# Kernel tuning notes

Hardware: AMD Instinct MI355X
Metric: run time of the kernel (lower is better)

## Reference

```python
import jax, jax.numpy as jnp
import numpy as np


def setup_inputs() -> dict:
    key = jax.random.key(0)
    k1, k2, k3, k4 = jax.random.split(key, 4)
    N, F, E = 100000, 128, 1600000
    Fo = F // 2
    x = jax.random.normal(k1, (N, F), dtype=jnp.float32)
    edge_index = jax.random.randint(k2, (2, E), 0, N, dtype=jnp.int32)
    W_conv = jax.random.normal(k3, (Fo, F), dtype=jnp.float32) * (1.0 / np.sqrt(F))
    b_conv = jnp.zeros((Fo,), dtype=jnp.float32)
    W_lin = jax.random.normal(k4, (1, Fo), dtype=jnp.float32) * (1.0 / np.sqrt(Fo))
    b_lin = jnp.zeros((1,), dtype=jnp.float32)
    return {"x": x, "edge_index": edge_index, "W_conv": W_conv,
            "b_conv": b_conv, "W_lin": W_lin, "b_lin": b_lin}


def gcn_conv(x, edge_index, W_conv, b_conv):
    # PyG GCNConv: add self-loops, symmetric normalization, x@W.T, scatter-add, + bias
    N = x.shape[0]
    loops = jnp.arange(N, dtype=edge_index.dtype)
    src = jnp.concatenate([edge_index[0], loops])  # message sources
    dst = jnp.concatenate([edge_index[1], loops])  # aggregation targets
    h = x @ W_conv.T  # [N, Fo]
    deg = jax.ops.segment_sum(jnp.ones_like(dst, dtype=h.dtype), dst, num_segments=N)
    dinv = jnp.where(deg > 0, jax.lax.rsqrt(deg), 0.0)
    norm = dinv[src] * dinv[dst]  # [E+N]
    msg = h[src] * norm[:, None]  # [E+N, Fo] -- dominant memory traffic
    agg = jax.ops.segment_sum(msg, dst, num_segments=N)
    return agg + b_conv


def reference(x, edge_index, W_conv, b_conv, W_lin, b_lin):
    h = gcn_conv(x, edge_index, W_conv, b_conv)
    h = jax.nn.relu(h)
    logits = h @ W_lin.T + b_lin  # [N, 1]
    return jax.nn.sigmoid(logits)
```

## Files before the change

kernel.cpp:

```cpp
#include <hip/hip_runtime.h>
#include <hip/hip_bf16.h>
#include <math.h>

#define F_IN   128
#define F_OUT  64
#define CHUNK  4096
#define EPT    16
#define BSH    7
#define CAP    3072
#define NBCA   1024

typedef short bf16x8 __attribute__((ext_vector_type(8)));
typedef float f32x4  __attribute__((ext_vector_type(4)));

__device__ __forceinline__ unsigned short f2bf(float f) {
    union { float f; unsigned int i; } c; c.f = f;
    unsigned int r = c.i + 0x7FFFu + ((c.i >> 16) & 1u);
    return (unsigned short)(r >> 16);
}
__device__ __forceinline__ unsigned int pk2bf(float a, float b) {
    __hip_bfloat162 p = __float22bfloat162_rn(make_float2(a, b));
    union { __hip_bfloat162 h; unsigned int u; } c; c.h = p; return c.u;
}
__device__ __forceinline__ float u_lo(unsigned int u) {
    union { unsigned int i; float f; } c; c.i = u << 16; return c.f;
}
__device__ __forceinline__ float u_hi(unsigned int u) {
    union { unsigned int i; float f; } c; c.i = u & 0xFFFF0000u; return c.f;
}

__global__ __launch_bounds__(256) void k_bin(
    const int* __restrict__ src, const int* __restrict__ dst, int E,
    unsigned int* __restrict__ bcnt, unsigned int* __restrict__ entries, int NBC) {
    __shared__ int hist[NBCA];
    __shared__ int gbase[NBCA];
    __shared__ int lcur[NBCA];
    const int tid = threadIdx.x;
    const int e0 = blockIdx.x * CHUNK;

    for (int c = tid; c < NBCA; c += 256) { hist[c] = 0; lcur[c] = 0; }
    __syncthreads();

    int dv[EPT], sv[EPT];
    #pragma unroll
    for (int j = 0; j < EPT; ++j) {
        int e = e0 + j * 256 + tid;
        if (e < E) {
            dv[j] = dst[e];
            sv[j] = src[e];
            atomicAdd(&hist[dv[j] >> BSH], 1);
        } else dv[j] = -1;
    }
    __syncthreads();

    for (int c = tid; c < NBC; c += 256) {
        int h = hist[c];
        gbase[c] = h ? (int)atomicAdd(&bcnt[c], (unsigned int)h) : 0;
    }
    __syncthreads();

    #pragma unroll
    for (int j = 0; j < EPT; ++j) {
        if (dv[j] >= 0) {
            int b = dv[j] >> BSH;
            int r = atomicAdd(&lcur[b], 1);
            entries[b * CAP + gbase[b] + r] =
                ((unsigned int)(dv[j] & 127) << 24) | (unsigned int)sv[j];
        }
    }
}

__global__ __launch_bounds__(256) void k_sort(
    const unsigned int* __restrict__ entries, const unsigned int* __restrict__ bcnt,
    int2* __restrict__ od, unsigned int* __restrict__ srcs, int N) {
    __shared__ unsigned int le[CAP];
    __shared__ unsigned int ls[CAP];
    __shared__ int hist[128];
    __shared__ int curs[128];
    const int tid = threadIdx.x;
    const int b = blockIdx.x;
    const int base = b * CAP;
    const int cnt = min((int)bcnt[b], CAP);

    if (tid < 128) hist[tid] = 0;
    __syncthreads();
    for (int i = tid; i < cnt; i += 256) {
        unsigned int v = entries[base + i];
        le[i] = v;
        atomicAdd(&hist[v >> 24], 1);
    }
    __syncthreads();

    int cntv = (tid < 128) ? hist[tid] : 0;
    if (tid < 128) curs[tid] = cntv;
    __syncthreads();
    for (int off = 1; off < 128; off <<= 1) {
        int t = (tid >= off && tid < 128) ? curs[tid - off] : 0;
        __syncthreads();
        if (tid < 128) curs[tid] += t;
        __syncthreads();
    }
    if (tid < 128) {
        int excl = curs[tid] - cntv;
        int d = (b << BSH) + tid;
        if (d < N) od[d] = make_int2(base + excl, cntv);
        curs[tid] = excl;
    }
    __syncthreads();

    for (int i = tid; i < cnt; i += 256) {
        unsigned int v = le[i];
        int p = atomicAdd(&curs[v >> 24], 1);
        ls[p] = (v & 0xFFFFFFu) << 7;
    }
    __syncthreads();

    for (int i = tid; i < cnt; i += 256)
        srcs[base + i] = ls[i];
}

__global__ __launch_bounds__(256) void k_gemm(
    const float* __restrict__ x, const float* __restrict__ W,
    const int2* __restrict__ od, unsigned short* __restrict__ g, int N) {
    __shared__ unsigned short xs[64 * F_IN];
    __shared__ unsigned short Wsh[F_OUT * F_IN];
    __shared__ float dinvs[64];

    const int tid  = threadIdx.x;
    const int row0 = blockIdx.x * 64;

    {
        const float4* W4 = (const float4*)W;
        #pragma unroll
        for (int t = 0; t < 8; ++t) {
            int idx = t * 256 + tid;
            float4 v = W4[idx];
            uint2 u = make_uint2(pk2bf(v.x, v.y), pk2bf(v.z, v.w));
            *(uint2*)&Wsh[idx * 4] = u;
        }
    }
    {
        const float4* x4 = (const float4*)x;
        #pragma unroll
        for (int t = 0; t < 8; ++t) {
            int idx = t * 256 + tid;
            int r = idx >> 5;
            int grow = row0 + r;
            float4 v = make_float4(0.f, 0.f, 0.f, 0.f);
            if (grow < N) v = x4[(size_t)grow * 32 + (idx & 31)];
            uint2 u = make_uint2(pk2bf(v.x, v.y), pk2bf(v.z, v.w));
            *(uint2*)&xs[idx * 4] = u;
        }
    }
    if (tid < 64) {
        int grow = row0 + tid;
        float dv = 1.0f;
        if (grow < N) dv = rsqrtf((float)od[grow].y + 1.0f);
        dinvs[tid] = dv;
    }
    __syncthreads();

    const int lane = tid & 63;
    const int wave = tid >> 6;
    const int m = lane & 15;
    const int q = lane >> 4;
    const int r0 = wave * 16;

    bf16x8 a[4];
    #pragma unroll
    for (int ks = 0; ks < 4; ++ks)
        a[ks] = *(const bf16x8*)&xs[(r0 + m) * F_IN + ks * 32 + q * 8];

    f32x4 acc[4] = {{0,0,0,0},{0,0,0,0},{0,0,0,0},{0,0,0,0}};
    #pragma unroll
    for (int ct = 0; ct < 4; ++ct) {
        #pragma unroll
        for (int ks = 0; ks < 4; ++ks) {
            bf16x8 b = *(const bf16x8*)&Wsh[(ct * 16 + m) * F_IN + ks * 32 + q * 8];
            acc[ct] = __builtin_amdgcn_mfma_f32_16x16x32_bf16(a[ks], b, acc[ct], 0, 0, 0);
        }
    }

    float dv[4];
    #pragma unroll
    for (int reg = 0; reg < 4; ++reg)
        dv[reg] = dinvs[r0 + q * 4 + reg];
    #pragma unroll
    for (int ct = 0; ct < 4; ++ct) {
        #pragma unroll
        for (int reg = 0; reg < 4; ++reg) {
            int grow = row0 + r0 + q * 4 + reg;
            if (grow <= N)
                g[(size_t)grow * F_OUT + ct * 16 + m] = f2bf(acc[ct][reg] * dv[reg]);
        }
    }
}

__global__ __launch_bounds__(256) void k_pull(
    const unsigned short* __restrict__ g, const int2* __restrict__ od,
    const unsigned int* __restrict__ srcs,
    const float* __restrict__ b_conv, const float* __restrict__ W_lin,
    const float* __restrict__ b_lin, float* __restrict__ out, int N) {
    const int lane = threadIdx.x & 63;
    const int li   = lane & 15;
    const int grp  = lane >> 4;
    const int wave   = (blockIdx.x * blockDim.x + threadIdx.x) >> 6;
    const int nwaves = (gridDim.x * blockDim.x) >> 6;

    const float4 wl = ((const float4*)W_lin)[li];
    const float4 bb = ((const float4*)b_conv)[li];
    const float  bl = b_lin[0];
    const char* gb = (const char*)g;
    const unsigned int lioff = ((unsigned int)li) << 3;
    const unsigned int sentb = ((unsigned int)N) << 7;

    for (int i = wave; i < N; i += nwaves) {
        int2 odv = od[i];
        int e0 = __builtin_amdgcn_readfirstlane(odv.x);
        int dg = __builtin_amdgcn_readfirstlane(odv.y);
        int full = dg >> 4;
        int rem  = dg & 15;

        uint2 us = *(const uint2*)(gb + ((((unsigned int)i) << 7) | lioff));
        float4 acc;
        acc.x = grp ? 0.f : u_lo(us.x);
        acc.y = grp ? 0.f : u_hi(us.x);
        acc.z = grp ? 0.f : u_lo(us.y);
        acc.w = grp ? 0.f : u_hi(us.y);

        const unsigned int* sp = srcs + e0 + grp;
        for (int it = 0; it < full; ++it) {
            unsigned int off[4];
            #pragma unroll
            for (int t = 0; t < 4; ++t)
                off[t] = sp[4 * t];
            uint2 u[4];
            #pragma unroll
            for (int t = 0; t < 4; ++t)
                u[t] = *(const uint2*)(gb + (size_t)(off[t] | lioff));
            #pragma unroll
            for (int t = 0; t < 4; ++t) {
                acc.x += u_lo(u[t].x); acc.y += u_hi(u[t].x);
                acc.z += u_lo(u[t].y); acc.w += u_hi(u[t].y);
            }
            sp += 16;
        }
        if (rem) {
            unsigned int off[4];
            #pragma unroll
            for (int t = 0; t < 4; ++t) {
                unsigned int o = sp[4 * t];
                off[t] = (4 * t + grp < rem) ? o : sentb;
            }
            uint2 u[4];
            #pragma unroll
            for (int t = 0; t < 4; ++t)
                u[t] = *(const uint2*)(gb + (size_t)(off[t] | lioff));
            #pragma unroll
            for (int t = 0; t < 4; ++t) {
                acc.x += u_lo(u[t].x); acc.y += u_hi(u[t].x);
                acc.z += u_lo(u[t].y); acc.w += u_hi(u[t].y);
            }
        }

        #pragma unroll
        for (int mk = 16; mk <= 32; mk <<= 1) {
            acc.x += __shfl_xor(acc.x, mk, 64);
            acc.y += __shfl_xor(acc.y, mk, 64);
            acc.z += __shfl_xor(acc.z, mk, 64);
            acc.w += __shfl_xor(acc.w, mk, 64);
        }

        float dinv = rsqrtf((float)dg + 1.0f);
        float r0 = fmaxf(acc.x * dinv + bb.x, 0.f);
        float r1 = fmaxf(acc.y * dinv + bb.y, 0.f);
        float r2 = fmaxf(acc.z * dinv + bb.z, 0.f);
        float r3 = fmaxf(acc.w * dinv + bb.w, 0.f);
        float t = r0 * wl.x + r1 * wl.y + r2 * wl.z + r3 * wl.w;
        #pragma unroll
        for (int mk = 1; mk <= 8; mk <<= 1)
            t += __shfl_xor(t, mk, 64);
        if (lane == 0)
            out[i] = 1.0f / (1.0f + expf(-(t + bl)));
    }
}

extern "C" void kernel_launch(void* const* d_in, const int* in_sizes, int n_in,
                              void* d_out, int out_size, void* d_ws, size_t ws_size,
                              hipStream_t stream) {
    const float* x      = (const float*)d_in[0];
    const int*   ei     = (const int*)d_in[1];
    const float* W_conv = (const float*)d_in[2];
    const float* b_conv = (const float*)d_in[3];
    const float* W_lin  = (const float*)d_in[4];
    const float* b_lin  = (const float*)d_in[5];

    const int N = in_sizes[0] / F_IN;
    const int E = in_sizes[1] / 2;
    const int* src = ei;
    const int* dst = ei + E;
    float* out = (float*)d_out;

    const int NBC  = (N + 127) >> BSH;
    const int NBLK = (E + CHUNK - 1) / CHUNK;
    const int Na   = NBC << BSH;

    unsigned int* bcnt = (unsigned int*)d_ws;
    int2* od = (int2*)(bcnt + NBCA);
    unsigned int* entries = (unsigned int*)((int*)od + 2 * Na);
    unsigned int* srcs = entries + (size_t)NBC * CAP;
    char* graw = (char*)(srcs + (size_t)NBC * CAP + 64);
    unsigned short* g = (unsigned short*)(((size_t)graw + 255) & ~(size_t)255);

    hipMemsetAsync(bcnt, 0, NBCA * 4, stream);
    k_bin  <<<NBLK, 256, 0, stream>>>(src, dst, E, bcnt, entries, NBC);
    k_sort <<<NBC, 256, 0, stream>>>(entries, bcnt, od, srcs, N);
    k_gemm <<<(N + 64) / 64, 256, 0, stream>>>(x, W_conv, od, g, N);
    k_pull <<<4096, 256, 0, stream>>>(g, od, srcs, b_conv, W_lin, b_lin, out, N);
}
```

Measured before the change: 175.9 us.

## Fuse bin, sort, gemm and pull stages into one cooperative persistent kernel

Merges the four separate launches into a single cooperative kernel that runs each stage as a grid-stride loop and separates stages with grid-wide barriers. It keeps the old multi-kernel path as a fallback if the cooperative launch fails. The binning chunk size is halved so the persistent grid spreads the work more evenly. The goal is to remove launch gaps and tail effects between kernels, at the cost of lower occupancy, grid-sync overhead and a single shared-memory footprint sized for the largest stage.

```diff
diff --git a/kernel.cpp b/kernel.cpp
--- a/kernel.cpp
+++ b/kernel.cpp
@@ -1,14 +1,17 @@
 #include <hip/hip_runtime.h>
+#include <hip/hip_cooperative_groups.h>
 #include <hip/hip_bf16.h>
 #include <math.h>
 
 #define F_IN   128
 #define F_OUT  64
-#define CHUNK  4096
-#define EPT    16
 #define BSH    7
 #define CAP    3072
-#define NBCA   1024
+#define CHUNK  2048
+#define EPT    8
+#define SMEM_SZ 33024
+
+namespace cg = cooperative_groups;
 
 typedef short bf16x8 __attribute__((ext_vector_type(8)));
 typedef float f32x4  __attribute__((ext_vector_type(4)));
@@ -29,174 +32,170 @@
     union { unsigned int i; float f; } c; c.i = u & 0xFFFF0000u; return c.f;
 }
 
-__global__ __launch_bounds__(256) void k_bin(
+__device__ __forceinline__ void dev_bin(
     const int* __restrict__ src, const int* __restrict__ dst, int E,
-    unsigned int* __restrict__ bcnt, unsigned int* __restrict__ entries, int NBC) {
-    __shared__ int hist[NBCA];
-    __shared__ int gbase[NBCA];
-    __shared__ int lcur[NBCA];
+    int NBC, int NCHUNK,
+    unsigned int* __restrict__ bcnt, unsigned int* __restrict__ entries,
+    char* smem) {
+    int* hist  = (int*)smem;
+    int* gbase = hist + 1024;
+    int* lcur  = gbase + 1024;
     const int tid = threadIdx.x;
-    const int e0 = blockIdx.x * CHUNK;
-
-    for (int c = tid; c < NBCA; c += 256) { hist[c] = 0; lcur[c] = 0; }
-    __syncthreads();
-
-    int dv[EPT], sv[EPT];
-    #pragma unroll
-    for (int j = 0; j < EPT; ++j) {
-        int e = e0 + j * 256 + tid;
-        if (e < E) {
-            dv[j] = dst[e];
-            sv[j] = src[e];
-            atomicAdd(&hist[dv[j] >> BSH], 1);
-        } else dv[j] = -1;
-    }
-    __syncthreads();
-
-    for (int c = tid; c < NBC; c += 256) {
-        int h = hist[c];
-        gbase[c] = h ? (int)atomicAdd(&bcnt[c], (unsigned int)h) : 0;
-    }
-    __syncthreads();
-
-    #pragma unroll
-    for (int j = 0; j < EPT; ++j) {
-        if (dv[j] >= 0) {
-            int b = dv[j] >> BSH;
-            int r = atomicAdd(&lcur[b], 1);
-            entries[b * CAP + gbase[b] + r] =
-                ((unsigned int)(dv[j] & 127) << 24) | (unsigned int)sv[j];
-        }
-    }
-}
-
-__global__ __launch_bounds__(256) void k_sort(
+    for (int c = blockIdx.x; c < NCHUNK; c += gridDim.x) {
+        for (int i = tid; i < 1024; i += 256) { hist[i] = 0; lcur[i] = 0; }
+        __syncthreads();
+        const int e0 = c * CHUNK;
+        int dv[EPT], sv[EPT];
+        #pragma unroll
+        for (int j = 0; j < EPT; ++j) {
+            int e = e0 + j * 256 + tid;
+            if (e < E) {
+                dv[j] = dst[e];
+                sv[j] = src[e];
+                atomicAdd(&hist[dv[j] >> BSH], 1);
+            } else dv[j] = -1;
+        }
+        __syncthreads();
+        for (int b = tid; b < NBC; b += 256) {
+            int h = hist[b];
+            gbase[b] = h ? (int)atomicAdd(&bcnt[b], (unsigned int)h) : 0;
+        }
+        __syncthreads();
+        #pragma unroll
+        for (int j = 0; j < EPT; ++j) {
+            if (dv[j] >= 0) {
+                int b = dv[j] >> BSH;
+                int r = atomicAdd(&lcur[b], 1);
+                entries[b * CAP + gbase[b] + r] =
+                    ((unsigned int)(dv[j] & 127) << 24) | (unsigned int)sv[j];
+            }
+        }
+        __syncthreads();
+    }
+}
+
+__device__ __forceinline__ void dev_sort(
     const unsigned int* __restrict__ entries, const unsigned int* __restrict__ bcnt,
-    int2* __restrict__ od, unsigned int* __restrict__ srcs, int N) {
-    __shared__ unsigned int le[CAP];
-    __shared__ unsigned int ls[CAP];
-    __shared__ int hist[128];
-    __shared__ int curs[128];
+    int2* __restrict__ od, unsigned int* __restrict__ srcs, int N, int NBC,
+    char* smem) {
+    unsigned int* le = (unsigned int*)smem;
+    unsigned int* ls = le + CAP;
+    int* hist = (int*)(ls + CAP);
+    int* curs = hist + 128;
     const int tid = threadIdx.x;
-    const int b = blockIdx.x;
-    const int base = b * CAP;
-    const int cnt = min((int)bcnt[b], CAP);
-
-    if (tid < 128) hist[tid] = 0;
-    __syncthreads();
-    for (int i = tid; i < cnt; i += 256) {
-        unsigned int v = entries[base + i];
-        le[i] = v;
-        atomicAdd(&hist[v >> 24], 1);
-    }
-    __syncthreads();
-
-    int cntv = (tid < 128) ? hist[tid] : 0;
-    if (tid < 128) curs[tid] = cntv;
-    __syncthreads();
-    for (int off = 1; off < 128; off <<= 1) {
-        int t = (tid >= off && tid < 128) ? curs[tid - off] : 0;
-        __syncthreads();
-        if (tid < 128) curs[tid] += t;
-        __syncthreads();
-    }
-    if (tid < 128) {
-        int excl = curs[tid] - cntv;
-        int d = (b << BSH) + tid;
-        if (d < N) od[d] = make_int2(base + excl, cntv);
-        curs[tid] = excl;
-    }
-    __syncthreads();
-
-    for (int i = tid; i < cnt; i += 256) {
-        unsigned int v = le[i];
-        int p = atomicAdd(&curs[v >> 24], 1);
-        ls[p] = (v & 0xFFFFFFu) << 7;
-    }
-    __syncthreads();
-
-    for (int i = tid; i < cnt; i += 256)
-        srcs[base + i] = ls[i];
-}
-
-__global__ __launch_bounds__(256) void k_gemm(
+    for (int b = blockIdx.x; b < NBC; b += gridDim.x) {
+        const int base = b * CAP;
+        const int cnt = min((int)bcnt[b], CAP);
+        if (tid < 128) hist[tid] = 0;
+        __syncthreads();
+        for (int i = tid; i < cnt; i += 256) {
+            unsigned int v = entries[base + i];
+            le[i] = v;
+            atomicAdd(&hist[v >> 24], 1);
+        }
+        __syncthreads();
+        int cntv = (tid < 128) ? hist[tid] : 0;
+        if (tid < 128) curs[tid] = cntv;
+        __syncthreads();
+        for (int off = 1; off < 128; off <<= 1) {
+            int t = (tid >= off && tid < 128) ? curs[tid - off] : 0;
+            __syncthreads();
+            if (tid < 128) curs[tid] += t;
+            __syncthreads();
+        }
+        if (tid < 128) {
+            int excl = curs[tid] - cntv;
+            int d = (b << BSH) + tid;
+            if (d < N) od[d] = make_int2(base + excl, cntv);
+            curs[tid] = excl;
+        }
+        __syncthreads();
+        for (int i = tid; i < cnt; i += 256) {
+            unsigned int v = le[i];
+            int p = atomicAdd(&curs[v >> 24], 1);
+            ls[p] = (v & 0xFFFFFFu) << 7;
+        }
+        __syncthreads();
+        for (int i = tid; i < cnt; i += 256)
+            srcs[base + i] = ls[i];
+        __syncthreads();
+    }
+}
+
+__device__ __forceinline__ void dev_gemm(
     const float* __restrict__ x, const float* __restrict__ W,
-    const int2* __restrict__ od, unsigned short* __restrict__ g, int N) {
-    __shared__ unsigned short xs[64 * F_IN];
-    __shared__ unsigned short Wsh[F_OUT * F_IN];
-    __shared__ float dinvs[64];
-
-    const int tid  = threadIdx.x;
-    const int row0 = blockIdx.x * 64;
-
+    const int2* __restrict__ od, unsigned short* __restrict__ g, int N, int NT,
+    char* smem) {
+    unsigned short* xs  = (unsigned short*)smem;
+    unsigned short* Wsh = xs + 64 * F_IN;
+    float* dinvs = (float*)(Wsh + F_OUT * F_IN);
+    const int tid = threadIdx.x;
     {
         const float4* W4 = (const float4*)W;
         #pragma unroll
         for (int t = 0; t < 8; ++t) {
             int idx = t * 256 + tid;
             float4 v = W4[idx];
-            uint2 u = make_uint2(pk2bf(v.x, v.y), pk2bf(v.z, v.w));
-            *(uint2*)&Wsh[idx * 4] = u;
-        }
-    }
-    {
-        const float4* x4 = (const float4*)x;
-        #pragma unroll
-        for (int t = 0; t < 8; ++t) {
-            int idx = t * 256 + tid;
-            int r = idx >> 5;
-            int grow = row0 + r;
-            float4 v = make_float4(0.f, 0.f, 0.f, 0.f);
-            if (grow < N) v = x4[(size_t)grow * 32 + (idx & 31)];
-            uint2 u = make_uint2(pk2bf(v.x, v.y), pk2bf(v.z, v.w));
-            *(uint2*)&xs[idx * 4] = u;
-        }
-    }
-    if (tid < 64) {
-        int grow = row0 + tid;
-        float dv = 1.0f;
-        if (grow < N) dv = rsqrtf((float)od[grow].y + 1.0f);
-        dinvs[tid] = dv;
-    }
-    __syncthreads();
-
+            *(uint2*)&Wsh[idx * 4] = make_uint2(pk2bf(v.x, v.y), pk2bf(v.z, v.w));
+        }
+    }
     const int lane = tid & 63;
-    const int wave = tid >> 6;
+    const int wv = tid >> 6;
     const int m = lane & 15;
     const int q = lane >> 4;
-    const int r0 = wave * 16;
-
-    bf16x8 a[4];
-    #pragma unroll
-    for (int ks = 0; ks < 4; ++ks)
-        a[ks] = *(const bf16x8*)&xs[(r0 + m) * F_IN + ks * 32 + q * 8];
-
-    f32x4 acc[4] = {{0,0,0,0},{0,0,0,0},{0,0,0,0},{0,0,0,0}};
-    #pragma unroll
-    for (int ct = 0; ct < 4; ++ct) {
-        #pragma unroll
-        for (int ks = 0; ks < 4; ++ks) {
-            bf16x8 b = *(const bf16x8*)&Wsh[(ct * 16 + m) * F_IN + ks * 32 + q * 8];
-            acc[ct] = __builtin_amdgcn_mfma_f32_16x16x32_bf16(a[ks], b, acc[ct], 0, 0, 0);
-        }
-    }
-
-    float dv[4];
-    #pragma unroll
-    for (int reg = 0; reg < 4; ++reg)
-        dv[reg] = dinvs[r0 + q * 4 + reg];
-    #pragma unroll
-    for (int ct = 0; ct < 4; ++ct) {
-        #pragma unroll
-        for (int reg = 0; reg < 4; ++reg) {
-            int grow = row0 + r0 + q * 4 + reg;
-            if (grow <= N)
-                g[(size_t)grow * F_OUT + ct * 16 + m] = f2bf(acc[ct][reg] * dv[reg]);
-        }
-    }
-}
-
-__global__ __launch_bounds__(256) void k_pull(
+    const int r0 = wv * 16;
+    for (int t0 = blockIdx.x; t0 < NT; t0 += gridDim.x) {
+        const int row0 = t0 * 64;
+        __syncthreads();
+        {
+            const float4* x4 = (const float4*)x;
+            #pragma unroll
+            for (int t = 0; t < 8; ++t) {
+                int idx = t * 256 + tid;
+                int r = idx >> 5;
+                int grow = row0 + r;
+                float4 v = make_float4(0.f, 0.f, 0.f, 0.f);
+                if (grow < N) v = x4[(size_t)grow * 32 + (idx & 31)];
+                *(uint2*)&xs[idx * 4] = make_uint2(pk2bf(v.x, v.y), pk2bf(v.z, v.w));
+            }
+        }
+        if (tid < 64) {
+            int grow = row0 + tid;
+            float dvv = 1.0f;
+            if (grow < N) dvv = rsqrtf((float)od[grow].y + 1.0f);
+            dinvs[tid] = dvv;
+        }
+        __syncthreads();
+        bf16x8 a[4];
+        #pragma unroll
+        for (int ks = 0; ks < 4; ++ks)
+            a[ks] = *(const bf16x8*)&xs[(r0 + m) * F_IN + ks * 32 + q * 8];
+        f32x4 acc[4] = {{0,0,0,0},{0,0,0,0},{0,0,0,0},{0,0,0,0}};
+        #pragma unroll
+        for (int ct = 0; ct < 4; ++ct) {
+            #pragma unroll
+            for (int ks = 0; ks < 4; ++ks) {
+                bf16x8 b = *(const bf16x8*)&Wsh[(ct * 16 + m) * F_IN + ks * 32 + q * 8];
+                acc[ct] = __builtin_amdgcn_mfma_f32_16x16x32_bf16(a[ks], b, acc[ct], 0, 0, 0);
+            }
+        }
+        float dvv[4];
+        #pragma unroll
+        for (int reg = 0; reg < 4; ++reg)
+            dvv[reg] = dinvs[r0 + q * 4 + reg];
+        #pragma unroll
+        for (int ct = 0; ct < 4; ++ct) {
+            #pragma unroll
+            for (int reg = 0; reg < 4; ++reg) {
+                int grow = row0 + r0 + q * 4 + reg;
+                if (grow <= N)
+                    g[(size_t)grow * F_OUT + ct * 16 + m] = f2bf(acc[ct][reg] * dvv[reg]);
+            }
+        }
+    }
+}
+
+__device__ __forceinline__ void dev_pull(
     const unsigned short* __restrict__ g, const int2* __restrict__ od,
     const unsigned int* __restrict__ srcs,
     const float* __restrict__ b_conv, const float* __restrict__ W_lin,
@@ -285,6 +284,55 @@
     }
 }
 
+__global__ __launch_bounds__(256, 4) void k_mega(
+    const float* __restrict__ x, const int* __restrict__ src, const int* __restrict__ dst,
+    const float* __restrict__ W, const float* __restrict__ b_conv,
+    const float* __restrict__ W_lin, const float* __restrict__ b_lin,
+    float* __restrict__ out, int N, int E, int NBC, int NCHUNK, int NT,
+    unsigned int* __restrict__ bcnt, int2* __restrict__ od,
+    unsigned int* __restrict__ entries, unsigned int* __restrict__ srcs,
+    unsigned short* __restrict__ g) {
+    __shared__ __align__(16) char smem[SMEM_SZ];
+    cg::grid_group grid = cg::this_grid();
+
+    dev_bin(src, dst, E, NBC, NCHUNK, bcnt, entries, smem);
+    __threadfence();
+    grid.sync();
+    dev_sort(entries, bcnt, od, srcs, N, NBC, smem);
+    __threadfence();
+    grid.sync();
+    dev_gemm(x, W, od, g, N, NT, smem);
+    __threadfence();
+    grid.sync();
+    dev_pull(g, od, srcs, b_conv, W_lin, b_lin, out, N);
+}
+
+__global__ __launch_bounds__(256) void k_binw(
+    const int* __restrict__ src, const int* __restrict__ dst, int E, int NBC,
+    int NCHUNK, unsigned int* __restrict__ bcnt, unsigned int* __restrict__ entries) {
+    __shared__ __align__(16) char smem[12288];
+    dev_bin(src, dst, E, NBC, NCHUNK, bcnt, entries, smem);
+}
+__global__ __launch_bounds__(256) void k_sortw(
+    const unsigned int* __restrict__ entries, const unsigned int* __restrict__ bcnt,
+    int2* __restrict__ od, unsigned int* __restrict__ srcs, int N, int NBC) {
+    __shared__ __align__(16) char smem[25600];
+    dev_sort(entries, bcnt, od, srcs, N, NBC, smem);
+}
+__global__ __launch_bounds__(256) void k_gemmw(
+    const float* __restrict__ x, const float* __restrict__ W,
+    const int2* __restrict__ od, unsigned short* __restrict__ g, int N, int NT) {
+    __shared__ __align__(16) char smem[SMEM_SZ];
+    dev_gemm(x, W, od, g, N, NT, smem);
+}
+__global__ __launch_bounds__(256) void k_pullw(
+    const unsigned short* __restrict__ g, const int2* __restrict__ od,
+    const unsigned int* __restrict__ srcs,
+    const float* __restrict__ b_conv, const float* __restrict__ W_lin,
+    const float* __restrict__ b_lin, float* __restrict__ out, int N) {
+    dev_pull(g, od, srcs, b_conv, W_lin, b_lin, out, N);
+}
+
 extern "C" void kernel_launch(void* const* d_in, const int* in_sizes, int n_in,
                               void* d_out, int out_size, void* d_ws, size_t ws_size,
                               hipStream_t stream) {
@@ -301,20 +349,40 @@
     const int* dst = ei + E;
     float* out = (float*)d_out;
 
-    const int NBC  = (N + 127) >> BSH;
-    const int NBLK = (E + CHUNK - 1) / CHUNK;
-    const int Na   = NBC << BSH;
+    const int NBC    = (N + 127) >> BSH;
+    const int NCHUNK = (E + CHUNK - 1) / CHUNK;
+    const int NT     = (N + 64) / 64;
+    const int Na     = NBC << BSH;
 
     unsigned int* bcnt = (unsigned int*)d_ws;
-    int2* od = (int2*)(bcnt + NBCA);
+    int2* od = (int2*)(bcnt + 1024);
     unsigned int* entries = (unsigned int*)((int*)od + 2 * Na);
     unsigned int* srcs = entries + (size_t)NBC * CAP;
     char* graw = (char*)(srcs + (size_t)NBC * CAP + 64);
     unsigned short* g = (unsigned short*)(((size_t)graw + 255) & ~(size_t)255);
 
-    hipMemsetAsync(bcnt, 0, NBCA * 4, stream);
-    k_bin  <<<NBLK, 256, 0, stream>>>(src, dst, E, bcnt, entries, NBC);
-    k_sort <<<NBC, 256, 0, stream>>>(entries, bcnt, od, srcs, N);
-    k_gemm <<<(N + 64) / 64, 256, 0, stream>>>(x, W_conv, od, g, N);
-    k_pull <<<4096, 256, 0, stream>>>(g, od, srcs, b_conv, W_lin, b_lin, out, N);
-}
+    hipMemsetAsync(bcnt, 0, 1024 * 4, stream);
+
+    int nb = 0;
+    if (hipOccupancyMaxActiveBlocksPerMultiprocessor(
+            &nb, (const void*)k_mega, 256, 0) != hipSuccess || nb <= 0)
+        nb = 3;
+    if (nb > 4) nb = 4;
+    int GB = nb * 256;
+
+    void* args[] = {
+        (void*)&x, (void*)&src, (void*)&dst, (void*)&W_conv, (void*)&b_conv,
+        (void*)&W_lin, (void*)&b_lin, (void*)&out, (void*)&N, (void*)&E,
+        (void*)&NBC, (void*)&NCHUNK, (void*)&NT, (void*)&bcnt, (void*)&od,
+        (void*)&entries, (void*)&srcs, (void*)&g };
+
+    hipError_t lerr = hipLaunchCooperativeKernel(
+        (const void*)k_mega, dim3(GB), dim3(256), args, 0, stream);
+    if (lerr != hipSuccess) {
+        (void)hipGetLastError();
+        k_binw <<<NCHUNK, 256, 0, stream>>>(src, dst, E, NBC, NCHUNK, bcnt, entries);
+        k_sortw<<<NBC, 256, 0, stream>>>(entries, bcnt, od, srcs, N, NBC);
+        k_gemmw<<<NT, 256, 0, stream>>>(x, W_conv, od, g, N, NT);
+        k_pullw<<<4096, 256, 0, stream>>>(g, od, srcs, b_conv, W_lin, b_lin, out, N);
+    }
+}
```

Result: slower. 676.9 us (+284.9%).
